# Optimization experiments

Measured on AMD Instinct MI355X. Metric: run time of the kernel, lower is better.

Reference implementation:

```python
import jax, jax.numpy as jnp
import numpy as np

D_MODEL = 1024
EXPAND = 2
D_INNER = EXPAND * D_MODEL          # 2048
D_STATE = 64
NGROUPS = 1
HEADDIM = 128
NHEADS = D_INNER // HEADDIM         # 16
D_CONV = 4
CONV_DIM = D_INNER + 2 * NGROUPS * D_STATE      # 2176
D_IN_PROJ = 2 * D_INNER + 2 * NGROUPS * D_STATE + NHEADS  # 4240
BATCH = 2
SEQLEN = 4096
RMS_EPS = 1e-5


def setup_inputs() -> dict:
    key = jax.random.key(0)
    ks = jax.random.split(key, 8)
    u = jax.random.normal(ks[0], (BATCH, SEQLEN, D_MODEL), jnp.float32)
    in_proj_w = jax.random.normal(ks[1], (D_IN_PROJ, D_MODEL), jnp.float32) * 0.02
    conv_w = jax.random.normal(ks[2], (CONV_DIM, D_CONV), jnp.float32) * 0.2
    conv_b = jax.random.normal(ks[3], (CONV_DIM,), jnp.float32) * 0.1
    dt_bias = jax.random.normal(ks[4], (NHEADS,), jnp.float32) * 0.5
    # A ~ Uniform(1,16), A_log = log(A)  (as in Mamba2 init)
    A_log = jnp.log(jax.random.uniform(ks[5], (NHEADS,), jnp.float32, 1.0, 16.0))
    D = jnp.ones((NHEADS,), jnp.float32)
    rms_w = jnp.ones((D_INNER,), jnp.float32)
    out_w = jax.random.normal(ks[6], (D_MODEL, D_INNER), jnp.float32) * 0.02
    return {"u": u, "in_proj_w": in_proj_w, "conv_w": conv_w, "conv_b": conv_b,
            "dt_bias": dt_bias, "A_log": A_log, "D": D, "rms_w": rms_w, "out_w": out_w}


def reference(u, in_proj_w, conv_w, conv_b, dt_bias, A_log, D, rms_w, out_w):
    Bsz, L, _ = u.shape
    # in_proj: (B,L,d_model) -> (B,L,d_in_proj), split [z, x, B, C, dt]
    zxbcdt = jnp.einsum('bld,ed->ble', u, in_proj_w)
    s1 = D_INNER
    s2 = 2 * D_INNER
    s3 = s2 + NGROUPS * D_STATE
    s4 = s3 + NGROUPS * D_STATE
    z = zxbcdt[..., :s1]
    x = zxbcdt[..., s1:s2]
    B_part = zxbcdt[..., s2:s3]
    C_part = zxbcdt[..., s3:s4]
    dt = zxbcdt[..., s4:]
    dt = jax.nn.softplus(dt + dt_bias)            # (B,L,H), dt_limit=(0,inf) -> no clamp

    # depthwise causal conv1d + silu over [x, B, C]
    xBC = jnp.concatenate([x, B_part, C_part], axis=-1)      # (B,L,CONV_DIM)
    xt = xBC.transpose(0, 2, 1)                              # (B,C,L)
    kern = conv_w[:, None, :]                                # (C,1,W)
    conv = jax.lax.conv_general_dilated(
        xt, kern, (1,), [(D_CONV - 1, 0)],
        dimension_numbers=('NCH', 'OIH', 'NCH'),
        feature_group_count=CONV_DIM)
    xBC = jax.nn.silu((conv + conv_b[None, :, None]).transpose(0, 2, 1))

    x_c = xBC[..., :D_INNER]
    B_c = xBC[..., D_INNER:D_INNER + NGROUPS * D_STATE]
    C_c = xBC[..., D_INNER + NGROUPS * D_STATE:]
    x_s = x_c.reshape(Bsz, L, NHEADS, HEADDIM)               # (B,L,H,P)
    hpg = NHEADS // NGROUPS
    B_full = jnp.repeat(B_c.reshape(Bsz, L, NGROUPS, D_STATE), hpg, axis=2)  # (B,L,H,N)
    C_full = jnp.repeat(C_c.reshape(Bsz, L, NGROUPS, D_STATE), hpg, axis=2)

    A = -jnp.exp(A_log)                                      # (H,)

    def step(state, inp):
        x_t, dt_t, B_t, C_t = inp  # (B,H,P),(B,H),(B,H,N),(B,H,N)
        decay = jnp.exp(dt_t * A)[:, :, None, None]          # (B,H,1,1)
        state = decay * state + B_t[:, :, None, :] * x_t[..., None]  # (B,H,P,N)
        y_t = jnp.einsum('bhpn,bhn->bhp', state, C_t)
        return state, y_t

    init = jnp.zeros((Bsz, NHEADS, HEADDIM, D_STATE), u.dtype)
    xs = (x_s.transpose(1, 0, 2, 3), dt.transpose(1, 0, 2),
          B_full.transpose(1, 0, 2, 3), C_full.transpose(1, 0, 2, 3))
    _, ys = jax.lax.scan(step, init, xs)                     # (L,B,H,P)
    y = ys.transpose(1, 0, 2, 3) + D[None, None, :, None] * x_s

    y_flat = y.reshape(Bsz, L, D_INNER)
    mu = jnp.mean(y_flat * y_flat, axis=-1, keepdims=True)
    y_flat = y_flat * jax.lax.rsqrt(mu + RMS_EPS) * rms_w    # RMSNorm
    y_flat = y_flat * jax.nn.sigmoid(z)                      # gate
    return jnp.einsum('bld,ed->ble', y_flat, out_w)          # out_proj (no bias)
```

## Files before the change

### kernel.cpp

```cpp
#include <hip/hip_runtime.h>
#include <math.h>

#define D_MODEL   1024
#define D_INNER   2048
#define D_STATE   64
#define HEADDIM   128
#define NHEADS    16
#define D_CONV    4
#define BATCH     2
#define SEQLEN    4096
#define RMS_EPS   1e-5f
#define D_IN_PROJ 4240

#define ZX_LD     4224

#define LCHUNK    128
#define NCHUNK    (SEQLEN / LCHUNK)

typedef __attribute__((ext_vector_type(8))) short short8;
typedef __attribute__((ext_vector_type(4))) float f32x4;

__device__ __forceinline__ ushort f2bf(float f) {
  unsigned u = __float_as_uint(f);
  u += 0x7fff + ((u >> 16) & 1);
  return (ushort)(u >> 16);
}
__device__ __forceinline__ float bf2f(ushort h) {
  return __uint_as_float(((unsigned)h) << 16);
}
__device__ __forceinline__ void ld4(const float* p, float* d) {
  float4 v = *(const float4*)p; d[0] = v.x; d[1] = v.y; d[2] = v.z; d[3] = v.w;
}
__device__ __forceinline__ void ld4b(const ushort* p, float* d) {
  ushort4 v = *(const ushort4*)p;
  d[0] = bf2f(v.x); d[1] = bf2f(v.y); d[2] = bf2f(v.z); d[3] = bf2f(v.w);
}

__device__ __forceinline__ void gl_lds16(const ushort* g, ushort* l) {
  __builtin_amdgcn_global_load_lds(
      (const __attribute__((address_space(1))) unsigned int*)g,
      (__attribute__((address_space(3))) unsigned int*)l, 16, 0, 0);
}

__global__ void cvt_split(const float* __restrict__ w,
                          ushort* __restrict__ hi, ushort* __restrict__ lo, int n4) {
  int i = blockIdx.x * 256 + threadIdx.x;
  if (i >= n4) return;
  float4 v = ((const float4*)w)[i];
  ushort h0 = f2bf(v.x), h1 = f2bf(v.y), h2 = f2bf(v.z), h3 = f2bf(v.w);
  ushort l0 = f2bf(v.x - bf2f(h0)), l1 = f2bf(v.y - bf2f(h1));
  ushort l2 = f2bf(v.z - bf2f(h2)), l3 = f2bf(v.w - bf2f(h3));
  ((ushort4*)hi)[i] = make_ushort4(h0, h1, h2, h3);
  ((ushort4*)lo)[i] = make_ushort4(l0, l1, l2, l3);
}

template<int BM, int BK, bool ALO, bool OBF16>
__launch_bounds__(256, 3)
__global__ void gemm_bf16p(const ushort* __restrict__ Ah, const ushort* __restrict__ Al,
                           const ushort* __restrict__ Bh, const ushort* __restrict__ Bl,
                           float* __restrict__ C, int ldc,
                           int M, int N, int ldab, int Kslice, int n1term) {
  constexpr int BN = 128;
  constexpr int NQ = BK / 8;
  constexpr int RT = BM / 32;
  constexpr int CT = 4;
  constexpr int KS = BK / 32;

  __shared__ ushort As[ALO ? 2 : 1][BM * BK];
  __shared__ ushort Bs[2][BN * BK];

  const int bn   = blockIdx.x * BN;
  if (bn >= N) return;
  const bool two = (bn >= n1term);
  const int t    = threadIdx.x;
  const int bm   = blockIdx.y * BM;
  const int kz   = blockIdx.z;
  const int kb   = kz * Kslice;
  C += (size_t)kz * M * ldc;
  const int wave = t >> 6, lane = t & 63;
  const int ml   = lane & 15, g4 = lane >> 4;
  const int sw   = ml & (NQ - 1);
  const int wr   = wave & 1, wc = wave >> 1;
  const int r0   = wr * RT * 16, c0 = wc * CT * 16;

  f32x4 acc[RT][CT];
#pragma unroll
  for (int i = 0; i < RT; ++i)
#pragma unroll
    for (int j = 0; j < CT; ++j) acc[i][j] = (f32x4){0.f, 0.f, 0.f, 0.f};

  for (int k0 = kb; k0 < kb + Kslice; k0 += BK) {
    __syncthreads();
#pragma unroll
    for (int ii = 0; ii < BM * NQ / 256; ++ii) {
      int idx = t + ii * 256;
      int row = idx / NQ, qs = idx % NQ;
      int qg  = qs ^ (row & (NQ - 1));
      size_t go = (size_t)(bm + row) * ldab + k0 + qg * 8;
      gl_lds16(Ah + go, &As[0][idx * 8]);
      if (ALO) gl_lds16(Al + go, &As[ALO ? 1 : 0][idx * 8]);
    }
#pragma unroll
    for (int ii = 0; ii < BN * NQ / 256; ++ii) {
      int idx = t + ii * 256;
      int row = idx / NQ, qs = idx % NQ;
      int qg  = qs ^ (row & (NQ - 1));
      size_t go = (size_t)(bn + row) * ldab + k0 + qg * 8;
      gl_lds16(Bh + go, &Bs[0][idx * 8]);
      if (two) gl_lds16(Bl + go, &Bs[1][idx * 8]);
    }
    __syncthreads();

#pragma unroll
    for (int ks = 0; ks < KS; ++ks) {
      const int qA = ((ks * 4 + g4) ^ sw) * 8;
      short8 ah[RT], al[RT], bh[CT], bl[CT];
#pragma unroll
      for (int i = 0; i < RT; ++i) {
        int off = (r0 + i * 16 + ml) * BK + qA;
        ah[i] = *(const short8*)&As[0][off];
        if (ALO) al[i] = *(const short8*)&As[ALO ? 1 : 0][off];
      }
#pragma unroll
      for (int j = 0; j < CT; ++j) {
        int off = (c0 + j * 16 + ml) * BK + qA;
        bh[j] = *(const short8*)&Bs[0][off];
        if (two) bl[j] = *(const short8*)&Bs[1][off];
      }
#pragma unroll
      for (int i = 0; i < RT; ++i)
#pragma unroll
        for (int j = 0; j < CT; ++j) {
          acc[i][j] = __builtin_amdgcn_mfma_f32_16x16x32_bf16(ah[i], bh[j], acc[i][j], 0, 0, 0);
          if (two)
            acc[i][j] = __builtin_amdgcn_mfma_f32_16x16x32_bf16(ah[i], bl[j], acc[i][j], 0, 0, 0);
          if (ALO)
            acc[i][j] = __builtin_amdgcn_mfma_f32_16x16x32_bf16(al[i], bh[j], acc[i][j], 0, 0, 0);
        }
    }
  }

#pragma unroll
  for (int i = 0; i < RT; ++i)
#pragma unroll
    for (int j = 0; j < CT; ++j) {
      int col = bn + c0 + j * 16 + ml;
      if (col < N) {
        int rowb = bm + r0 + i * 16 + g4 * 4;
#pragma unroll
        for (int r = 0; r < 4; ++r) {
          if (OBF16) ((ushort*)C)[(size_t)(rowb + r) * ldc + col] = f2bf(acc[i][j][r]);
          else       C[(size_t)(rowb + r) * ldc + col] = acc[i][j][r];
        }
      }
    }
}

__global__ void add_out(const float* __restrict__ P, float* __restrict__ out, int n4) {
  int i = blockIdx.x * 256 + threadIdx.x;
  if (i >= n4) return;
  float4 a = ((const float4*)P)[i];
  float4 b = ((const float4*)(P + (size_t)SEQLEN * D_MODEL))[i];
  ((float4*)out)[i] = make_float4(a.x + b.x, a.y + b.y, a.z + b.z, a.w + b.w);
}

__global__ void add_dt(const float* __restrict__ P, float* __restrict__ dtb) {
  int i = blockIdx.x * 256 + threadIdx.x;
  if (i >= SEQLEN * NHEADS / 4) return;
  float4 s = ((const float4*)P)[i];
#pragma unroll
  for (int k = 1; k < 8; ++k) {
    float4 v = ((const float4*)(P + (size_t)k * SEQLEN * NHEADS))[i];
    s.x += v.x; s.y += v.y; s.z += v.z; s.w += v.w;
  }
  ((float4*)dtb)[i] = s;
}


__device__ __forceinline__ void cum_scan(float* cum, float v, int t, float* carry) {
  int lane = t & 63;
#pragma unroll
  for (int off = 1; off < 64; off <<= 1) {
    float o = __shfl_up(v, off);
    if (lane >= off) v += o;
  }
  if (t == 63) *carry = v;
  __syncthreads();
  if (t >= 64 && t < LCHUNK) v += *carry;
  if (t < LCHUNK) cum[t] = v;
  __syncthreads();
}

__device__ __forceinline__ void conv4b(const ushort* __restrict__ zx,
                                       const float* __restrict__ cw,
                                       const float* __restrict__ cb,
                                       int l, int col0, float* outv) {
  const ushort* bp = zx + (size_t)l * ZX_LD + col0;
  float r3[4], r2[4], r1[4], r0[4], bb[4];
  ld4b(bp, r3);
  if (l >= 1) ld4b(bp - ZX_LD, r2);     else { r2[0]=r2[1]=r2[2]=r2[3]=0.f; }
  if (l >= 2) ld4b(bp - 2 * ZX_LD, r1); else { r1[0]=r1[1]=r1[2]=r1[3]=0.f; }
  if (l >= 3) ld4b(bp - 3 * ZX_LD, r0); else { r0[0]=r0[1]=r0[2]=r0[3]=0.f; }
  const int ch = col0 - 2048;
  ld4(cb + ch, bb);
#pragma unroll
  for (int j = 0; j < 4; ++j) {
    float w4[4]; ld4(cw + (ch + j) * 4, w4);
    float a = bb[j];
    a = fmaf(w4[0], r0[j], a);
    a = fmaf(w4[1], r1[j], a);
    a = fmaf(w4[2], r2[j], a);
    a = fmaf(w4[3], r3[j], a);
    outv[j] = a / (1.f + __expf(-a));
  }
}

__launch_bounds__(256, 2)
__global__ void passA_ssd(const ushort* __restrict__ zx,
                          const float* __restrict__ dtb,
                          const float* __restrict__ cw, const float* __restrict__ cb,
                          const float* __restrict__ dt_bias,
                          const float* __restrict__ A_log,
                          float* __restrict__ Sc, float* __restrict__ Pc,
                          float* __restrict__ xconv, float* __restrict__ bconv) {
  const int blk = blockIdx.x;
  const int c   = blk & (NCHUNK - 1);
  const int h   = blk >> 5;
  const int l0  = c * LCHUNK;
  const int t   = threadIdx.x;
  const int wave = t >> 6, lane = t & 63;
  const int ml = lane & 15, g4 = lane >> 4;
  const float Ah = -expf(A_log[h]);

  __shared__ float cum[LCHUNK];
  __shared__ float carry;
  __shared__ ushort Xt[2][LCHUNK * 40];
  __shared__ ushort Bt[2][D_STATE * 40];

  {
    float v = 0.f;
    if (t < LCHUNK) {
      float xv = dtb[(size_t)(l0 + t) * NHEADS + h] + dt_bias[h];
      float sp = (xv > 20.f) ? xv : log1pf(expf(xv));
      v = sp * Ah;
    }
    cum_scan(cum, v, t, &carry);
  }
  const float cend = cum[LCHUNK - 1];

  f32x4 acc[2][4];
#pragma unroll
  for (int i = 0; i < 2; ++i)
#pragma unroll
    for (int j = 0; j < 4; ++j) acc[i][j] = (f32x4){0.f, 0.f, 0.f, 0.f};
  const int p0 = wave * 32;

  for (int slab = 0; slab < 4; ++slab) {
    __syncthreads();
    for (int i = 0; i < 4; ++i) {
      int q = t + i * 256;
      int s = q >> 5, p4 = (q & 31) * 4;
      int l = l0 + slab * 32 + s;
      float xv[4];
      conv4b(zx, cw, cb, l, 2048 + h * HEADDIM + p4, xv);
      *(float4*)(xconv + (size_t)l * D_INNER + h * HEADDIM + p4) =
          make_float4(xv[0], xv[1], xv[2], xv[3]);
#pragma unroll
      for (int j = 0; j < 4; ++j) {
        ushort hh = f2bf(xv[j]);
        Xt[0][(p4 + j) * 40 + s] = hh;
        Xt[1][(p4 + j) * 40 + s] = f2bf(xv[j] - bf2f(hh));
      }
    }
    for (int i = 0; i < 2; ++i) {
      int q = t + i * 256;
      int s = q >> 4, n4 = (q & 15) * 4;
      int l = l0 + slab * 32 + s;
      float wd = __expf(cend - cum[slab * 32 + s]);
      float bv[4];
      conv4b(zx, cw, cb, l, 4096 + n4, bv);
      if (h == 0)
        *(float4*)(bconv + (size_t)l * D_STATE + n4) =
            make_float4(bv[0], bv[1], bv[2], bv[3]);
#pragma unroll
      for (int j = 0; j < 4; ++j) {
        float val = bv[j] * wd;
        ushort hh = f2bf(val);
        Bt[0][(n4 + j) * 40 + s] = hh;
        Bt[1][(n4 + j) * 40 + s] = f2bf(val - bf2f(hh));
      }
    }
    __syncthreads();

    short8 xa_h[2], xa_l[2];
#pragma unroll
    for (int pi = 0; pi < 2; ++pi) {
      int off = (p0 + pi * 16 + ml) * 40 + g4 * 8;
      xa_h[pi] = *(const short8*)&Xt[0][off];
      xa_l[pi] = *(const short8*)&Xt[1][off];
    }
#pragma unroll
    for (int ni = 0; ni < 4; ++ni) {
      int off = (ni * 16 + ml) * 40 + g4 * 8;
      short8 bh = *(const short8*)&Bt[0][off];
      short8 bl = *(const short8*)&Bt[1][off];
#pragma unroll
      for (int pi = 0; pi < 2; ++pi) {
        acc[pi][ni] = __builtin_amdgcn_mfma_f32_16x16x32_bf16(xa_h[pi], bh, acc[pi][ni], 0, 0, 0);
        acc[pi][ni] = __builtin_amdgcn_mfma_f32_16x16x32_bf16(xa_h[pi], bl, acc[pi][ni], 0, 0, 0);
        acc[pi][ni] = __builtin_amdgcn_mfma_f32_16x16x32_bf16(xa_l[pi], bh, acc[pi][ni], 0, 0, 0);
      }
    }
  }

  float* S = Sc + (size_t)blk * (HEADDIM * D_STATE);
#pragma unroll
  for (int pi = 0; pi < 2; ++pi)
#pragma unroll
    for (int ni = 0; ni < 4; ++ni) {
      int n = ni * 16 + ml;
#pragma unroll
      for (int r = 0; r < 4; ++r) {
        int p = p0 + pi * 16 + g4 * 4 + r;
        S[(size_t)p * D_STATE + n] = acc[pi][ni][r];
      }
    }
  if (t == 0) Pc[blk] = __expf(cend);
}

__global__ void scan_passB(float* __restrict__ Sc, const float* __restrict__ Pc) {
  const int h = blockIdx.x;
  const int e = blockIdx.y * 512 + threadIdx.x;
  const size_t hb = (size_t)h * NCHUNK;
  float st = 0.f;
  for (int c = 0; c < NCHUNK; ++c) {
    size_t idx = (hb + c) * (HEADDIM * D_STATE) + e;
    float P = Pc[hb + c];
    float v = Sc[idx];
    Sc[idx] = st;
    st = fmaf(P, st, v);
  }
}

__launch_bounds__(256, 2)
__global__ void passC_ssd(const ushort* __restrict__ zx,
                          const float* __restrict__ dtb,
                          const float* __restrict__ cw, const float* __restrict__ cb,
                          const float* __restrict__ dt_bias,
                          const float* __restrict__ A_log,
                          const float* __restrict__ Dp,
                          const float* __restrict__ Sc,
                          const float* __restrict__ bconv,
                          float* __restrict__ ybuf) {
  const int blk = blockIdx.x;
  const int c   = blk & (NCHUNK - 1);
  const int h   = blk >> 5;
  const int l0  = c * LCHUNK;
  const int t   = threadIdx.x;
  const int wave = t >> 6, lane = t & 63;
  const int ml = lane & 15, g4 = lane >> 4;
  const int t0 = wave * 32;
  const float Ah = -expf(A_log[h]);
  const float Dh = Dp[h];

  __shared__ float cum[LCHUNK];
  __shared__ float carry;
  __shared__ ushort Bsl[2][2][32 * 40];
  __shared__ ushort Msl[2][LCHUNK * 40];
  __shared__ ushort Xt[2][LCHUNK * 40];

  {
    float v = 0.f;
    if (t < LCHUNK) {
      float xv = dtb[(size_t)(l0 + t) * NHEADS + h] + dt_bias[h];
      float sp = (xv > 20.f) ? xv : log1pf(expf(xv));
      v = sp * Ah;
    }
    cum_scan(cum, v, t, &carry);
  }

  short8 c_h[2][2], c_l[2][2];
  {
    ushort* CSh = &Msl[0][0];
    ushort* CSl = &Xt[0][0];
    int row = t >> 1, half = t & 1;
    int l = l0 + row;
    int colbase = 4160 + half * 32;
#pragma unroll
    for (int j0 = 0; j0 < 32; j0 += 4) {
      float cv[4];
      conv4b(zx, cw, cb, l, colbase + j0, cv);
      int colc = half * 32 + j0;
      int quad = colc >> 3;
      int addr = row * 64 + ((quad ^ (row & 7)) << 3) + (colc & 7);
      ushort h0 = f2bf(cv[0]), h1 = f2bf(cv[1]), h2 = f2bf(cv[2]), h3 = f2bf(cv[3]);
      *(ushort4*)&CSh[addr] = make_ushort4(h0, h1, h2, h3);
      *(ushort4*)&CSl[addr] = make_ushort4(
          f2bf(cv[0] - bf2f(h0)), f2bf(cv[1] - bf2f(h1)),
          f2bf(cv[2] - bf2f(h2)), f2bf(cv[3] - bf2f(h3)));
    }
    __syncthreads();
#pragma unroll
    for (int ks = 0; ks < 2; ++ks)
#pragma unroll
      for (int ti = 0; ti < 2; ++ti) {
        int rw = t0 + ti * 16 + ml;
        int ad = rw * 64 + (((ks * 4 + g4) ^ (rw & 7)) << 3);
        c_h[ks][ti] = *(const short8*)&CSh[ad];
        c_l[ks][ti] = *(const short8*)&CSl[ad];
      }
  }

  f32x4 accY[2][8];
#pragma unroll
  for (int i = 0; i < 2; ++i)
#pragma unroll
    for (int j = 0; j < 8; ++j) accY[i][j] = (f32x4){0.f, 0.f, 0.f, 0.f};

  const float* xcv = ybuf;

  for (int slab = 0; slab < 4; ++slab) {
    __syncthreads();
#pragma unroll
    for (int i = 0; i < 2; ++i) {
      int q = t + i * 256;
      int s = q >> 4, n4 = (q & 15) * 4;
      int l = l0 + slab * 32 + s;
      float4 v = *(const float4*)(bconv + (size_t)l * D_STATE + n4);
      float bv[4] = {v.x, v.y, v.z, v.w};
      int ks = n4 >> 5, jj = n4 & 31;
      ushort h0 = f2bf(bv[0]), h1 = f2bf(bv[1]), h2 = f2bf(bv[2]), h3 = f2bf(bv[3]);
      *(ushort4*)&Bsl[ks][0][s * 40 + jj] = make_ushort4(h0, h1, h2, h3);
      *(ushort4*)&Bsl[ks][1][s * 40 + jj] = make_ushort4(
          f2bf(bv[0] - bf2f(h0)), f2bf(bv[1] - bf2f(h1)),
          f2bf(bv[2] - bf2f(h2)), f2bf(bv[3] - bf2f(h3)));
    }
#pragma unroll
    for (int i = 0; i < 4; ++i) {
      int q = t + i * 256;
      int p = q & 127, sg = q >> 7;
      ushort hh[4], ll[4];
#pragma unroll
      for (int j = 0; j < 4; ++j) {
        int l = l0 + slab * 32 + sg * 4 + j;
        float xv = xcv[(size_t)l * D_INNER + h * HEADDIM + p];
        hh[j] = f2bf(xv);
        ll[j] = f2bf(xv - bf2f(hh[j]));
      }
      *(ushort4*)&Xt[0][p * 40 + sg * 4] = make_ushort4(hh[0], hh[1], hh[2], hh[3]);
      *(ushort4*)&Xt[1][p * 40 + sg * 4] = make_ushort4(ll[0], ll[1], ll[2], ll[3]);
    }
    __syncthreads();

    if (wave >= slab) {
      f32x4 g[2][2];
#pragma unroll
      for (int i = 0; i < 2; ++i)
#pragma unroll
        for (int j = 0; j < 2; ++j) g[i][j] = (f32x4){0.f, 0.f, 0.f, 0.f};
#pragma unroll
      for (int ks = 0; ks < 2; ++ks) {
#pragma unroll
        for (int si = 0; si < 2; ++si) {
          int off = (si * 16 + ml) * 40 + g4 * 8;
          short8 bh = *(const short8*)&Bsl[ks][0][off];
          short8 bl = *(const short8*)&Bsl[ks][1][off];
#pragma unroll
          for (int ti = 0; ti < 2; ++ti) {
            g[ti][si] = __builtin_amdgcn_mfma_f32_16x16x32_bf16(c_h[ks][ti], bh, g[ti][si], 0, 0, 0);
            g[ti][si] = __builtin_amdgcn_mfma_f32_16x16x32_bf16(c_h[ks][ti], bl, g[ti][si], 0, 0, 0);
            g[ti][si] = __builtin_amdgcn_mfma_f32_16x16x32_bf16(c_l[ks][ti], bh, g[ti][si], 0, 0, 0);
          }
        }
      }
#pragma unroll
      for (int ti = 0; ti < 2; ++ti)
#pragma unroll
        for (int si = 0; si < 2; ++si) {
          int sl = si * 16 + ml;
          int sg = slab * 32 + sl;
#pragma unroll
          for (int r = 0; r < 4; ++r) {
            int tg = t0 + ti * 16 + g4 * 4 + r;
            float coeff = (sg <= tg) ? __expf(cum[tg] - cum[sg]) : 0.f;
            float val = g[ti][si][r] * coeff + ((sg == tg) ? Dh : 0.f);
            ushort hh = f2bf(val);
            Msl[0][tg * 40 + sl] = hh;
            Msl[1][tg * 40 + sl] = f2bf(val - bf2f(hh));
          }
        }
      asm volatile("s_waitcnt lgkmcnt(0)" ::: "memory");
      short8 ma_h[2], ma_l[2];
#pragma unroll
      for (int ti = 0; ti < 2; ++ti) {
        int off = (t0 + ti * 16 + ml) * 40 + g4 * 8;
        ma_h[ti] = *(const short8*)&Msl[0][off];
        ma_l[ti] = *(const short8*)&Msl[1][off];
      }
#pragma unroll
      for (int pi = 0; pi < 8; ++pi) {
        int off = (pi * 16 + ml) * 40 + g4 * 8;
        short8 xh = *(const short8*)&Xt[0][off];
        short8 xl = *(const short8*)&Xt[1][off];
#pragma unroll
        for (int ti = 0; ti < 2; ++ti) {
          accY[ti][pi] = __builtin_amdgcn_mfma_f32_16x16x32_bf16(ma_h[ti], xh, accY[ti][pi], 0, 0, 0);
          accY[ti][pi] = __builtin_amdgcn_mfma_f32_16x16x32_bf16(ma_h[ti], xl, accY[ti][pi], 0, 0, 0);
          accY[ti][pi] = __builtin_amdgcn_mfma_f32_16x16x32_bf16(ma_l[ti], xh, accY[ti][pi], 0, 0, 0);
        }
      }
    }
  }

  const float* S = Sc + (size_t)blk * (HEADDIM * D_STATE);
#pragma unroll
  for (int ns = 0; ns < 2; ++ns) {
    __syncthreads();
#pragma unroll
    for (int i = 0; i < 4; ++i) {
      int q = t + i * 256;
      int p = q >> 3, j4 = (q & 7) * 4;
      float4 v = *(const float4*)(S + (size_t)p * D_STATE + ns * 32 + j4);
      float vv[4] = {v.x, v.y, v.z, v.w};
      ushort hh0 = f2bf(vv[0]), hh1 = f2bf(vv[1]), hh2 = f2bf(vv[2]), hh3 = f2bf(vv[3]);
      *(ushort4*)&Xt[0][p * 40 + j4] = make_ushort4(hh0, hh1, hh2, hh3);
      *(ushort4*)&Xt[1][p * 40 + j4] =
          make_ushort4(f2bf(vv[0] - bf2f(hh0)), f2bf(vv[1] - bf2f(hh1)),
                       f2bf(vv[2] - bf2f(hh2)), f2bf(vv[3] - bf2f(hh3)));
    }
    __syncthreads();
    short8 ma_h[2], ma_l[2];
#pragma unroll
    for (int ti = 0; ti < 2; ++ti) {
      float e = __expf(cum[t0 + ti * 16 + ml]);
#pragma unroll
      for (int j = 0; j < 8; ++j) {
        float v = (bf2f((ushort)c_h[ns][ti][j]) + bf2f((ushort)c_l[ns][ti][j])) * e;
        ushort hh = f2bf(v);
        ma_h[ti][j] = (short)hh;
        ma_l[ti][j] = (short)f2bf(v - bf2f(hh));
      }
    }
#pragma unroll
    for (int pi = 0; pi < 8; ++pi) {
      int off = (pi * 16 + ml) * 40 + g4 * 8;
      short8 xh = *(const short8*)&Xt[0][off];
      short8 xl = *(const short8*)&Xt[1][off];
#pragma unroll
      for (int ti = 0; ti < 2; ++ti) {
        accY[ti][pi] = __builtin_amdgcn_mfma_f32_16x16x32_bf16(ma_h[ti], xh, accY[ti][pi], 0, 0, 0);
        accY[ti][pi] = __builtin_amdgcn_mfma_f32_16x16x32_bf16(ma_h[ti], xl, accY[ti][pi], 0, 0, 0);
        accY[ti][pi] = __builtin_amdgcn_mfma_f32_16x16x32_bf16(ma_l[ti], xh, accY[ti][pi], 0, 0, 0);
      }
    }
  }

#pragma unroll
  for (int ti = 0; ti < 2; ++ti)
#pragma unroll
    for (int pi = 0; pi < 8; ++pi) {
      int p = pi * 16 + ml;
#pragma unroll
      for (int r = 0; r < 4; ++r) {
        int l = l0 + t0 + ti * 16 + g4 * 4 + r;
        ybuf[(size_t)l * D_INNER + h * HEADDIM + p] = accY[ti][pi][r];
      }
    }
}

__launch_bounds__(256)
__global__ void rmsnorm_gate_split(const float* __restrict__ ybuf,
                                   const ushort* __restrict__ zx,
                                   const float* __restrict__ rms_w,
                                   ushort* __restrict__ yh) {
  const int row = blockIdx.x;
  const int t   = threadIdx.x;
  const float* y  = ybuf + (size_t)row * D_INNER;
  const ushort* z = zx   + (size_t)row * ZX_LD;

  float4 a  = *(const float4*)(y + t * 8);
  float4 bq = *(const float4*)(y + t * 8 + 4);
  float ss = a.x * a.x + a.y * a.y + a.z * a.z + a.w * a.w +
             bq.x * bq.x + bq.y * bq.y + bq.z * bq.z + bq.w * bq.w;
#pragma unroll
  for (int off = 32; off > 0; off >>= 1) ss += __shfl_down(ss, off);
  __shared__ float red[4];
  if ((t & 63) == 0) red[t >> 6] = ss;
  __syncthreads();
  float tot = red[0] + red[1] + red[2] + red[3];
  float scale = rsqrtf(tot * (1.f / (float)D_INNER) + RMS_EPS);

  float vy[8] = {a.x, a.y, a.z, a.w, bq.x, bq.y, bq.z, bq.w};
  ushort4 zv0 = *(const ushort4*)(z + t * 8);
  ushort4 zv1 = *(const ushort4*)(z + t * 8 + 4);
  ushort zz[8] = {zv0.x, zv0.y, zv0.z, zv0.w, zv1.x, zv1.y, zv1.z, zv1.w};
  ushort hh[8];
#pragma unroll
  for (int jj = 0; jj < 8; ++jj) {
    int col = t * 8 + jj;
    float g = 1.f / (1.f + __expf(-bf2f(zz[jj])));
    float v = vy[jj] * scale * rms_w[col] * g;
    hh[jj] = f2bf(v);
  }
  size_t o = (size_t)row * D_INNER + t * 8;
  *(ushort4*)(yh + o)     = make_ushort4(hh[0], hh[1], hh[2], hh[3]);
  *(ushort4*)(yh + o + 4) = make_ushort4(hh[4], hh[5], hh[6], hh[7]);
}

extern "C" void kernel_launch(void* const* d_in, const int* in_sizes, int n_in,
                              void* d_out, int out_size, void* d_ws, size_t ws_size,
                              hipStream_t stream) {
  const float* u         = (const float*)d_in[0];
  const float* in_proj_w = (const float*)d_in[1];
  const float* conv_w    = (const float*)d_in[2];
  const float* conv_b    = (const float*)d_in[3];
  const float* dt_bias   = (const float*)d_in[4];
  const float* A_log     = (const float*)d_in[5];
  const float* Dp        = (const float*)d_in[6];
  const float* rms_w     = (const float*)d_in[7];
  const float* out_w     = (const float*)d_in[8];
  float* out = (float*)d_out;

  float* ws    = (float*)d_ws;
  ushort* zxbc = (ushort*)ws;
  float* dtb   = ws   + (size_t)SEQLEN * ZX_LD / 2;
  float* dtp   = dtb  + (size_t)SEQLEN * NHEADS;
  float* ybuf  = dtp  + (size_t)8 * SEQLEN * NHEADS;
  float* Pc    = ybuf + (size_t)SEQLEN * D_INNER;
  float* Sc    = Pc   + 512;
  ushort* uh   = (ushort*)(Sc + (size_t)NHEADS * NCHUNK * HEADDIM * D_STATE);
  ushort* ul   = uh  + (size_t)SEQLEN * D_MODEL;
  ushort* w1h  = ul  + (size_t)SEQLEN * D_MODEL;
  ushort* w1l  = w1h + (size_t)D_IN_PROJ * D_MODEL;
  ushort* w2h  = w1l + (size_t)D_IN_PROJ * D_MODEL;
  ushort* w2l  = w2h + (size_t)D_MODEL * D_INNER;
  ushort* yh   = (ushort*)Sc;
  float* Opart = ybuf;
  float* bconv = dtp;

  {
    int n4 = D_IN_PROJ * D_MODEL / 4;
    cvt_split<<<(n4 + 255) / 256, 256, 0, stream>>>(in_proj_w, w1h, w1l, n4);
    int m4 = D_MODEL * D_INNER / 4;
    cvt_split<<<(m4 + 255) / 256, 256, 0, stream>>>(out_w, w2h, w2l, m4);
  }

  for (int b = 0; b < BATCH; ++b) {
    const float* u_b  = u   + (size_t)b * SEQLEN * D_MODEL;
    float*      out_b = out + (size_t)b * SEQLEN * D_MODEL;

    {
      int n4 = SEQLEN * D_MODEL / 4;
      cvt_split<<<(n4 + 255) / 256, 256, 0, stream>>>(u_b, uh, ul, n4);
    }

    {
      dim3 g(40, SEQLEN / 128, 1);
      gemm_bf16p<128, 64, false, true><<<g, 256, 0, stream>>>(uh, uh, w1h, w1l,
                                                          (float*)zxbc, ZX_LD, SEQLEN,
                                                          ZX_LD, D_MODEL, D_MODEL,
                                                          D_INNER);
    }
    {
      const ushort* bh = w1h + (size_t)ZX_LD * D_MODEL;
      const ushort* bl = w1l + (size_t)ZX_LD * D_MODEL;
      dim3 g(1, SEQLEN / 128, 8);
      gemm_bf16p<128, 32, true, false><<<g, 256, 0, stream>>>(uh, ul, bh, bl,
                                                          dtp, NHEADS, SEQLEN, NHEADS,
                                                          D_MODEL, D_MODEL / 8, 0);
      add_dt<<<(SEQLEN * NHEADS / 4 + 255) / 256, 256, 0, stream>>>(dtp, dtb);
    }

    passA_ssd<<<NHEADS * NCHUNK, 256, 0, stream>>>(zxbc, dtb, conv_w, conv_b,
                                                   dt_bias, A_log, Sc, Pc,
                                                   ybuf, bconv);
    scan_passB<<<dim3(NHEADS, (HEADDIM * D_STATE) / 512), 512, 0, stream>>>(Sc, Pc);
    passC_ssd<<<NHEADS * NCHUNK, 256, 0, stream>>>(zxbc, dtb, conv_w, conv_b,
                                                   dt_bias, A_log, Dp, Sc,
                                                   bconv, ybuf);

    rmsnorm_gate_split<<<SEQLEN, 256, 0, stream>>>(ybuf, zxbc, rms_w, yh);

    {
      dim3 g(D_MODEL / 128, SEQLEN / 128, 2);
      gemm_bf16p<128, 64, false, false><<<g, 256, 0, stream>>>(yh, yh, w2h, w2l,
                                                           Opart, D_MODEL, SEQLEN, D_MODEL,
                                                           D_INNER, D_INNER / 2, 0);
    }
    add_out<<<(SEQLEN * D_MODEL / 4 + 255) / 256, 256, 0, stream>>>(Opart, out_b,
                                                                    SEQLEN * D_MODEL / 4);
  }
}
```

Baseline: 536.8 us.

## Double-buffer LDS tiles in bf16 split GEMM with explicit vmcnt waits

Restructures the GEMM main loop so the global-to-LDS loads for tile k+2 are issued while tile k is being computed. Two LDS buffers are used, with hand-placed s_waitcnt vmcnt counts sized to the number of outstanding loads per stage. BK drops from 64 to 32 for the in_proj and out_proj launches so the doubled LDS footprint still fits three blocks per CU. The cost is more loop iterations and barriers, plus hand-coded wait counts that must match the per-stage load count exactly.

```diff
diff --git a/kernel.cpp b/kernel.cpp
--- a/kernel.cpp
+++ b/kernel.cpp
@@ -65,9 +65,10 @@
   constexpr int RT = BM / 32;
   constexpr int CT = 4;
   constexpr int KS = BK / 32;
-
-  __shared__ ushort As[ALO ? 2 : 1][BM * BK];
-  __shared__ ushort Bs[2][BN * BK];
+  constexpr int APL = ALO ? 2 : 1;
+
+  __shared__ ushort As[2][APL][BM * BK];
+  __shared__ ushort Bs[2][2][BN * BK];
 
   const int bn   = blockIdx.x * BN;
   if (bn >= N) return;
@@ -89,16 +90,17 @@
 #pragma unroll
     for (int j = 0; j < CT; ++j) acc[i][j] = (f32x4){0.f, 0.f, 0.f, 0.f};
 
-  for (int k0 = kb; k0 < kb + Kslice; k0 += BK) {
-    __syncthreads();
+  const int NIT = Kslice / BK;
+
+  auto stage = [&](int k0, int buf) {
 #pragma unroll
     for (int ii = 0; ii < BM * NQ / 256; ++ii) {
       int idx = t + ii * 256;
       int row = idx / NQ, qs = idx % NQ;
       int qg  = qs ^ (row & (NQ - 1));
       size_t go = (size_t)(bm + row) * ldab + k0 + qg * 8;
-      gl_lds16(Ah + go, &As[0][idx * 8]);
-      if (ALO) gl_lds16(Al + go, &As[ALO ? 1 : 0][idx * 8]);
+      gl_lds16(Ah + go, &As[buf][0][idx * 8]);
+      if (ALO) gl_lds16(Al + go, &As[buf][APL - 1][idx * 8]);
     }
 #pragma unroll
     for (int ii = 0; ii < BN * NQ / 256; ++ii) {
@@ -106,10 +108,25 @@
       int row = idx / NQ, qs = idx % NQ;
       int qg  = qs ^ (row & (NQ - 1));
       size_t go = (size_t)(bn + row) * ldab + k0 + qg * 8;
-      gl_lds16(Bh + go, &Bs[0][idx * 8]);
-      if (two) gl_lds16(Bl + go, &Bs[1][idx * 8]);
-    }
-    __syncthreads();
+      gl_lds16(Bh + go, &Bs[buf][0][idx * 8]);
+      if (two) gl_lds16(Bl + go, &Bs[buf][1][idx * 8]);
+    }
+  };
+
+  stage(kb, 0);
+  if (NIT > 1) stage(kb + BK, 1);
+
+  for (int it = 0; it < NIT; ++it) {
+    const int buf = it & 1;
+    if (it + 1 < NIT) {
+      if (ALO && two)        asm volatile("s_waitcnt vmcnt(8)" ::: "memory");
+      else if (ALO || two)   asm volatile("s_waitcnt vmcnt(6)" ::: "memory");
+      else                   asm volatile("s_waitcnt vmcnt(4)" ::: "memory");
+    } else {
+      asm volatile("s_waitcnt vmcnt(0)" ::: "memory");
+    }
+    __builtin_amdgcn_s_barrier();
+    __builtin_amdgcn_sched_barrier(0);
 
 #pragma unroll
     for (int ks = 0; ks < KS; ++ks) {
@@ -118,14 +135,14 @@
 #pragma unroll
       for (int i = 0; i < RT; ++i) {
         int off = (r0 + i * 16 + ml) * BK + qA;
-        ah[i] = *(const short8*)&As[0][off];
-        if (ALO) al[i] = *(const short8*)&As[ALO ? 1 : 0][off];
+        ah[i] = *(const short8*)&As[buf][0][off];
+        if (ALO) al[i] = *(const short8*)&As[buf][APL - 1][off];
       }
 #pragma unroll
       for (int j = 0; j < CT; ++j) {
         int off = (c0 + j * 16 + ml) * BK + qA;
-        bh[j] = *(const short8*)&Bs[0][off];
-        if (two) bl[j] = *(const short8*)&Bs[1][off];
+        bh[j] = *(const short8*)&Bs[buf][0][off];
+        if (two) bl[j] = *(const short8*)&Bs[buf][1][off];
       }
 #pragma unroll
       for (int i = 0; i < RT; ++i)
@@ -138,6 +155,11 @@
             acc[i][j] = __builtin_amdgcn_mfma_f32_16x16x32_bf16(al[i], bh[j], acc[i][j], 0, 0, 0);
         }
     }
+
+    __builtin_amdgcn_sched_barrier(0);
+    __builtin_amdgcn_s_barrier();
+    __builtin_amdgcn_sched_barrier(0);
+    if (it + 2 < NIT) stage(kb + (size_t)(it + 2) * BK, buf);
   }
 
 #pragma unroll
@@ -656,7 +678,7 @@
 
     {
       dim3 g(40, SEQLEN / 128, 1);
-      gemm_bf16p<128, 64, false, true><<<g, 256, 0, stream>>>(uh, uh, w1h, w1l,
+      gemm_bf16p<128, 32, false, true><<<g, 256, 0, stream>>>(uh, uh, w1h, w1l,
                                                           (float*)zxbc, ZX_LD, SEQLEN,
                                                           ZX_LD, D_MODEL, D_MODEL,
                                                           D_INNER);
@@ -683,7 +705,7 @@
 
     {
       dim3 g(D_MODEL / 128, SEQLEN / 128, 2);
-      gemm_bf16p<128, 64, false, false><<<g, 256, 0, stream>>>(yh, yh, w2h, w2l,
+      gemm_bf16p<128, 32, false, false><<<g, 256, 0, stream>>>(yh, yh, w2h, w2l,
                                                            Opart, D_MODEL, SEQLEN, D_MODEL,
                                                            D_INNER, D_INNER / 2, 0);
     }
```

New measurement: 588.3 us. +9.6%, slower.

## Switch in_proj and out_proj GEMMs from split-bf16 to single-term fp16 MFMA

Applied to the files above, without the earlier changes.

Adds an fp16 GEMM kernel that uses one MFMA per tile instead of the bf16 hi/lo split terms. It converts u, the z/x/B/C rows of in_proj_w and out_w to fp16, and the normalised-gated activation now feeds the out projection in fp16. This removes the extra low-part MFMAs and loads in the two large projections, trading them for fp16 rounding that has more mantissa than a single bf16 term. The dt slice still uses the split bf16 path. The change adds conversion passes and reuses ybuf as scratch for the fp16 copy of u, and fp16 carries overflow and range risk.

```diff
diff --git a/kernel.cpp b/kernel.cpp
--- a/kernel.cpp
+++ b/kernel.cpp
@@ -19,6 +19,7 @@
 
 typedef __attribute__((ext_vector_type(8))) short short8;
 typedef __attribute__((ext_vector_type(4))) float f32x4;
+typedef _Float16 half8 __attribute__((ext_vector_type(8)));
 
 __device__ __forceinline__ ushort f2bf(float f) {
   unsigned u = __float_as_uint(f);
@@ -27,6 +28,10 @@
 }
 __device__ __forceinline__ float bf2f(ushort h) {
   return __uint_as_float(((unsigned)h) << 16);
+}
+__device__ __forceinline__ ushort f2h(float f) {
+  _Float16 h = (_Float16)f;
+  ushort u; __builtin_memcpy(&u, &h, 2); return u;
 }
 __device__ __forceinline__ void ld4(const float* p, float* d) {
   float4 v = *(const float4*)p; d[0] = v.x; d[1] = v.y; d[2] = v.z; d[3] = v.w;
@@ -52,6 +57,13 @@
   ushort l2 = f2bf(v.z - bf2f(h2)), l3 = f2bf(v.w - bf2f(h3));
   ((ushort4*)hi)[i] = make_ushort4(h0, h1, h2, h3);
   ((ushort4*)lo)[i] = make_ushort4(l0, l1, l2, l3);
+}
+
+__global__ void cvt_f16(const float* __restrict__ w, ushort* __restrict__ o, int n4) {
+  int i = blockIdx.x * 256 + threadIdx.x;
+  if (i >= n4) return;
+  float4 v = ((const float4*)w)[i];
+  ((ushort4*)o)[i] = make_ushort4(f2h(v.x), f2h(v.y), f2h(v.z), f2h(v.w));
 }
 
 template<int BM, int BK, bool ALO, bool OBF16>
@@ -137,6 +149,93 @@
           if (ALO)
             acc[i][j] = __builtin_amdgcn_mfma_f32_16x16x32_bf16(al[i], bh[j], acc[i][j], 0, 0, 0);
         }
+    }
+  }
+
+#pragma unroll
+  for (int i = 0; i < RT; ++i)
+#pragma unroll
+    for (int j = 0; j < CT; ++j) {
+      int col = bn + c0 + j * 16 + ml;
+      if (col < N) {
+        int rowb = bm + r0 + i * 16 + g4 * 4;
+#pragma unroll
+        for (int r = 0; r < 4; ++r) {
+          if (OBF16) ((ushort*)C)[(size_t)(rowb + r) * ldc + col] = f2bf(acc[i][j][r]);
+          else       C[(size_t)(rowb + r) * ldc + col] = acc[i][j][r];
+        }
+      }
+    }
+}
+
+template<int BM, int BK, bool OBF16>
+__launch_bounds__(256, 4)
+__global__ void gemm_f16(const ushort* __restrict__ Ah, const ushort* __restrict__ Bh,
+                         float* __restrict__ C, int ldc,
+                         int M, int N, int ldab, int Kslice) {
+  constexpr int BN = 128;
+  constexpr int NQ = BK / 8;
+  constexpr int RT = BM / 32;
+  constexpr int CT = 4;
+  constexpr int KS = BK / 32;
+
+  __shared__ ushort As[BM * BK];
+  __shared__ ushort Bs[BN * BK];
+
+  const int bn   = blockIdx.x * BN;
+  if (bn >= N) return;
+  const int t    = threadIdx.x;
+  const int bm   = blockIdx.y * BM;
+  const int kz   = blockIdx.z;
+  const int kb   = kz * Kslice;
+  C += (size_t)kz * M * ldc;
+  const int wave = t >> 6, lane = t & 63;
+  const int ml   = lane & 15, g4 = lane >> 4;
+  const int sw   = ml & (NQ - 1);
+  const int wr   = wave & 1, wc = wave >> 1;
+  const int r0   = wr * RT * 16, c0 = wc * CT * 16;
+
+  f32x4 acc[RT][CT];
+#pragma unroll
+  for (int i = 0; i < RT; ++i)
+#pragma unroll
+    for (int j = 0; j < CT; ++j) acc[i][j] = (f32x4){0.f, 0.f, 0.f, 0.f};
+
+  for (int k0 = kb; k0 < kb + Kslice; k0 += BK) {
+    __syncthreads();
+#pragma unroll
+    for (int ii = 0; ii < BM * NQ / 256; ++ii) {
+      int idx = t + ii * 256;
+      int row = idx / NQ, qs = idx % NQ;
+      int qg  = qs ^ (row & (NQ - 1));
+      size_t go = (size_t)(bm + row) * ldab + k0 + qg * 8;
+      gl_lds16(Ah + go, &As[idx * 8]);
+    }
+#pragma unroll
+    for (int ii = 0; ii < BN * NQ / 256; ++ii) {
+      int idx = t + ii * 256;
+      int row = idx / NQ, qs = idx % NQ;
+      int qg  = qs ^ (row & (NQ - 1));
+      size_t go = (size_t)(bn + row) * ldab + k0 + qg * 8;
+      gl_lds16(Bh + go, &Bs[idx * 8]);
+    }
+    __syncthreads();
+
+#pragma unroll
+    for (int ks = 0; ks < KS; ++ks) {
+      const int qA = ((ks * 4 + g4) ^ sw) * 8;
+      half8 ah[RT], bh[CT];
+#pragma unroll
+      for (int i = 0; i < RT; ++i)
+        ah[i] = *(const half8*)&As[(r0 + i * 16 + ml) * BK + qA];
+#pragma unroll
+      for (int j = 0; j < CT; ++j)
+        bh[j] = *(const half8*)&Bs[(c0 + j * 16 + ml) * BK + qA];
+#pragma unroll
+      for (int i = 0; i < RT; ++i)
+#pragma unroll
+        for (int j = 0; j < CT; ++j)
+          acc[i][j] = __builtin_amdgcn_mfma_f32_16x16x32_f16(ah[i], bh[j], acc[i][j], 0, 0, 0);
     }
   }
 
@@ -600,7 +699,7 @@
     int col = t * 8 + jj;
     float g = 1.f / (1.f + __expf(-bf2f(zz[jj])));
     float v = vy[jj] * scale * rms_w[col] * g;
-    hh[jj] = f2bf(v);
+    hh[jj] = f2h(v);
   }
   size_t o = (size_t)row * D_INNER + t * 8;
   *(ushort4*)(yh + o)     = make_ushort4(hh[0], hh[1], hh[2], hh[3]);
@@ -637,12 +736,15 @@
   ushort* yh   = (ushort*)Sc;
   float* Opart = ybuf;
   float* bconv = dtp;
+  ushort* uf16 = (ushort*)ybuf;
 
   {
     int n4 = D_IN_PROJ * D_MODEL / 4;
     cvt_split<<<(n4 + 255) / 256, 256, 0, stream>>>(in_proj_w, w1h, w1l, n4);
+    int z4 = ZX_LD * D_MODEL / 4;
+    cvt_f16<<<(z4 + 255) / 256, 256, 0, stream>>>(in_proj_w, w1h, z4);
     int m4 = D_MODEL * D_INNER / 4;
-    cvt_split<<<(m4 + 255) / 256, 256, 0, stream>>>(out_w, w2h, w2l, m4);
+    cvt_f16<<<(m4 + 255) / 256, 256, 0, stream>>>(out_w, w2h, m4);
   }
 
   for (int b = 0; b < BATCH; ++b) {
@@ -652,14 +754,14 @@
     {
       int n4 = SEQLEN * D_MODEL / 4;
       cvt_split<<<(n4 + 255) / 256, 256, 0, stream>>>(u_b, uh, ul, n4);
+      cvt_f16<<<(n4 + 255) / 256, 256, 0, stream>>>(u_b, uf16, n4);
     }
 
     {
       dim3 g(40, SEQLEN / 128, 1);
-      gemm_bf16p<128, 64, false, true><<<g, 256, 0, stream>>>(uh, uh, w1h, w1l,
-                                                          (float*)zxbc, ZX_LD, SEQLEN,
-                                                          ZX_LD, D_MODEL, D_MODEL,
-                                                          D_INNER);
+      gemm_f16<128, 64, true><<<g, 256, 0, stream>>>(uf16, w1h, (float*)zxbc,
+                                                     ZX_LD, SEQLEN, ZX_LD,
+                                                     D_MODEL, D_MODEL);
     }
     {
       const ushort* bh = w1h + (size_t)ZX_LD * D_MODEL;
@@ -683,9 +785,9 @@
 
     {
       dim3 g(D_MODEL / 128, SEQLEN / 128, 2);
-      gemm_bf16p<128, 64, false, false><<<g, 256, 0, stream>>>(yh, yh, w2h, w2l,
-                                                           Opart, D_MODEL, SEQLEN, D_MODEL,
-                                                           D_INNER, D_INNER / 2, 0);
+      gemm_f16<128, 64, false><<<g, 256, 0, stream>>>(yh, w2h, Opart, D_MODEL,
+                                                      SEQLEN, D_MODEL,
+                                                      D_INNER, D_INNER / 2);
     }
     add_out<<<(SEQLEN * D_MODEL / 4 + 255) / 256, 256, 0, stream>>>(Opart, out_b,
                                                                     SEQLEN * D_MODEL / 4);
```

Result: faster. 518.8 us (-3.4%).
